# Kernel optimization log

Hardware: AMD Instinct MI355X
Metric: run time of the kernel (lower is better)

Reference implementation:

```python
import jax, jax.numpy as jnp
import numpy as np

WS = 8          # window size
NH = 16         # num heads
C = 256         # in_channels
L = WS * WS     # tokens per window
EPS = 1e-5      # LayerNorm eps

def _rel_index():
    coords = np.stack(np.meshgrid(np.arange(WS), np.arange(WS), indexing='ij')).reshape(2, -1)
    rel = coords[:, :, None] - coords[:, None, :]
    rel = rel + (WS - 1)
    rel[0] = rel[0] * (2 * WS - 1)
    return jnp.asarray(rel.sum(0))  # [L, L] int

REL_IDX = _rel_index()

def _ln(x, g, b):
    m = x.mean(-1, keepdims=True)
    v = jnp.var(x, axis=-1, keepdims=True)
    return (x - m) * jax.lax.rsqrt(v + EPS) * g + b

def setup_inputs() -> dict:
    key = jax.random.key(0)
    ks = jax.random.split(key, 8)
    return {
        'x': jax.random.normal(ks[0], (2, C, 256, 256), dtype=jnp.float32),
        'pre_gamma': jnp.ones((C,), jnp.float32),
        'pre_beta': jnp.zeros((C,), jnp.float32),
        'post_gamma': jnp.ones((C,), jnp.float32),
        'post_beta': jnp.zeros((C,), jnp.float32),
        'qkv_w': jax.random.normal(ks[1], (C, 3 * C), jnp.float32) * 0.02,
        'qkv_b': jnp.zeros((3 * C,), jnp.float32),
        'proj_w': jax.random.normal(ks[2], (C, C), jnp.float32) * 0.02,
        'proj_b': jnp.zeros((C,), jnp.float32),
        'rel_bias_table': jax.random.normal(ks[3], ((2 * WS - 1) ** 2, NH), jnp.float32) * 0.02,
    }

def reference(x, pre_gamma, pre_beta, post_gamma, post_beta, qkv_w, qkv_b, proj_w, proj_b, rel_bias_table):
    N, Cc, H, W = x.shape
    # block partition: [N,C,H,W] -> [N*nWin, L, C]
    t = x.reshape(N, Cc, H // WS, WS, W // WS, WS)
    t = t.transpose(0, 2, 4, 3, 5, 1).reshape(-1, L, Cc)
    B = t.shape[0]
    # pre-norm + relative self-attention (cosine / normalized qk)
    y = _ln(t, pre_gamma, pre_beta)
    qkv = (y @ qkv_w + qkv_b).reshape(B, L, 3, NH, Cc // NH).transpose(2, 0, 3, 1, 4)
    q, k, v = qkv[0], qkv[1], qkv[2]  # [B, h, L, dh]
    q = q / jnp.maximum(jnp.linalg.norm(q, axis=-1, keepdims=True), 1e-12)
    k = k / jnp.maximum(jnp.linalg.norm(k, axis=-1, keepdims=True), 1e-12)
    bias = rel_bias_table[REL_IDX].transpose(2, 0, 1)  # [h, L, L]
    attn = jax.nn.softmax(jnp.einsum('bhld,bhmd->bhlm', q, k) + bias, axis=-1)
    o = jnp.einsum('bhlm,bhmd->bhld', attn, v).transpose(0, 2, 1, 3).reshape(B, L, Cc)
    o = o @ proj_w + proj_b
    out = t + o
    # post-norm residual (mlp is Identity in MetNet-3)
    out = out + _ln(out, post_gamma, post_beta)
    # reverse partition -> [N, C, H, W]
    out = out.reshape(N, H // WS, W // WS, WS, WS, Cc)
    out = out.transpose(0, 5, 1, 3, 2, 4).reshape(N, Cc, H, W)
    return out
```

## Files before the change

kernel.cpp:

```cpp
#include <hip/hip_runtime.h>


#define WSZ 8
#define LTOK 64
#define NH 16
#define CCH 256
#define WW2 256
#define HWP 65536
#define NWIN 2048

#define TP 258
#define QP2 18
#define VP2 66
#define PP2 66
#define OHP 36

typedef __bf16 bf16x8 __attribute__((ext_vector_type(8)));
typedef float  f32x4  __attribute__((ext_vector_type(4)));
typedef unsigned short u16;
typedef uint4  __attribute__((may_alias)) uint4_a;
typedef float4 __attribute__((may_alias)) float4_a;

__device__ __forceinline__ float b2f(u16 u) {
    return (float)__builtin_bit_cast(__bf16, u);
}
__device__ __forceinline__ u16 f2b(float f) {
    return __builtin_bit_cast(u16, (__bf16)f);
}
__device__ __forceinline__ __bf16 u2b(u16 u) {
    return __builtin_bit_cast(__bf16, u);
}
__device__ __forceinline__ float gload(const void* p, int idx, int isf32) {
    return isf32 ? ((const float*)p)[idx] : b2f(((const u16*)p)[idx]);
}

static __global__ void detect_dtype(const u16* __restrict__ xu, int* __restrict__ flag) {
    int lane = threadIdx.x;
    u16 u = xu[lane];
    int e = (u >> 7) & 0xFF;
    bool plaus = (u == 0) || (e >= 0x6C && e <= 0x86);
    unsigned long long m = __ballot(plaus);
    if (lane == 0) flag[0] = (__popcll(m) >= 56) ? 0 : 1;
}

static __global__ __launch_bounds__(256) void prep_qkv(
        const void* __restrict__ qkv_w, const void* __restrict__ qkv_b,
        const void* __restrict__ g, const void* __restrict__ be,
        u16* __restrict__ gwT, float* __restrict__ D2, float* __restrict__ D3,
        const int* __restrict__ flagp)
{
    const int isf32 = flagp[0];
    int col = blockIdx.x;
    int c   = threadIdx.x;
    float gv = gload(g, c, isf32), bv = gload(be, c, isf32);
    float wv = gload(qkv_w, c * 768 + col, isf32);
    gwT[col * 256 + c] = f2b(gv * wv);
    float s2 = gv * wv, s3 = bv * wv;
    #pragma unroll
    for (int off = 32; off; off >>= 1) {
        s2 += __shfl_xor(s2, off);
        s3 += __shfl_xor(s3, off);
    }
    __shared__ float p2[4], p3[4];
    int wvid = threadIdx.x >> 6, ln = threadIdx.x & 63;
    if (ln == 0) { p2[wvid] = s2; p3[wvid] = s3; }
    __syncthreads();
    if (threadIdx.x == 0) {
        D2[col] = p2[0] + p2[1] + p2[2] + p2[3];
        D3[col] = p3[0] + p3[1] + p3[2] + p3[3] + gload(qkv_b, col, isf32);
    }
}

static __global__ __launch_bounds__(256) void prep_proj(
        const void* __restrict__ proj_w, u16* __restrict__ pwT,
        const void* __restrict__ table, float* __restrict__ tablef,
        const int* __restrict__ flagp)
{
    const int isf32 = flagp[0];
    int nrow = blockIdx.x, k = threadIdx.x;
    pwT[nrow * 256 + k] = f2b(gload(proj_w, k * 256 + nrow, isf32));
    int gid = blockIdx.x * 256 + threadIdx.x;
    if (gid < (2 * WSZ - 1) * (2 * WSZ - 1) * NH)
        tablef[gid] = gload(table, gid, isf32);
}

static __global__ __launch_bounds__(256, 3) void win_attn(
    const void* __restrict__ x, void* __restrict__ out,
    const u16* __restrict__ gwT, const u16* __restrict__ pwT,
    const float* __restrict__ D2, const float* __restrict__ D3,
    const void* __restrict__ proj_b, const void* __restrict__ postg,
    const void* __restrict__ postb, const float* __restrict__ tablef,
    const int* __restrict__ flagp)
{
    __shared__ u16 sm_t[LTOK * TP];
    __shared__ u16 sm_q[LTOK * QP2];
    __shared__ u16 sm_k[LTOK * QP2];
    __shared__ u16 sm_vt[NH * VP2];
    __shared__ u16 sm_p[LTOK * PP2];
    __shared__ u16 sm_oh[LTOK * OHP];
    __shared__ float sm_mean[LTOK], sm_rstd[LTOK];
    __shared__ u16 sm_zero[16];

    const int isf32 = flagp[0];
    const int tid  = threadIdx.x;
    const int wv   = tid >> 6;
    const int lane = tid & 63;
    const int quad = lane >> 4;
    const int n15  = lane & 15;

    const int b0 = blockIdx.x;
    const int b  = ((b0 & 7) << 8) | (b0 >> 3);
    const int nb = b >> 10, wh = (b >> 5) & 31, wwi = b & 31;
    const int base = nb * (CCH * HWP) + wh * (8 * WW2) + wwi * 8;

    if (tid < 16) sm_zero[tid] = 0;

    if (isf32) {
        const float* xf = (const float*)x;
        #pragma unroll
        for (int r = 0; r < 8; ++r) {
            int s = tid + r * 256;
            int c = s >> 3, i = s & 7;
            const float* src = xf + base + c * HWP + i * WW2;
            float4 a = *(const float4_a*)(src);
            float4 d = *(const float4_a*)(src + 4);
            u16* dst = &sm_t[(i * 8) * TP + c];
            dst[0 * TP] = f2b(a.x);  dst[1 * TP] = f2b(a.y);
            dst[2 * TP] = f2b(a.z);  dst[3 * TP] = f2b(a.w);
            dst[4 * TP] = f2b(d.x);  dst[5 * TP] = f2b(d.y);
            dst[6 * TP] = f2b(d.z);  dst[7 * TP] = f2b(d.w);
        }
    } else {
        const u16* xu = (const u16*)x;
        #pragma unroll
        for (int r = 0; r < 8; ++r) {
            int s = tid + r * 256;
            int c = s >> 3, i = s & 7;
            const uint4 v = *(const uint4_a*)(xu + base + c * HWP + i * WW2);
            u16* dst = &sm_t[(i * 8) * TP + c];
            dst[0 * TP] = (u16)(v.x & 0xffff);  dst[1 * TP] = (u16)(v.x >> 16);
            dst[2 * TP] = (u16)(v.y & 0xffff);  dst[3 * TP] = (u16)(v.y >> 16);
            dst[4 * TP] = (u16)(v.z & 0xffff);  dst[5 * TP] = (u16)(v.z >> 16);
            dst[6 * TP] = (u16)(v.w & 0xffff);  dst[7 * TP] = (u16)(v.w >> 16);
        }
    }
    __syncthreads();

    {
        int l = tid >> 2, g = tid & 3;
        float s = 0.f, ss = 0.f;
        const u16* row = &sm_t[l * TP + g * 64];
        #pragma unroll
        for (int e = 0; e < 64; ++e) {
            float a = b2f(row[e]);
            s += a; ss += a * a;
        }
        s += __shfl_xor(s, 1); ss += __shfl_xor(ss, 1);
        s += __shfl_xor(s, 2); ss += __shfl_xor(ss, 2);
        if (g == 0) {
            float mean = s * (1.f / 256.f);
            float var  = ss * (1.f / 256.f) - mean * mean;
            sm_mean[l] = mean;
            sm_rstd[l] = rsqrtf(var + 1e-5f);
        }
    }

    float s4[4], ms4[4];
    #pragma unroll
    for (int r = 0; r < 4; ++r) {
        int tok = wv * 16 + quad * 4 + r;
        float mu = sm_mean[tok], sd = sm_rstd[tok];
        s4[r] = sd; ms4[r] = -mu * sd;
    }

    bf16x8 afr[8];
    {
        const u16* arow = &sm_t[(wv * 16 + n15) * TP];
        #pragma unroll
        for (int kb = 0; kb < 8; ++kb) {
            #pragma unroll
            for (int j = 0; j < 8; ++j)
                afr[kb][j] = u2b(arow[kb * 32 + quad * 8 + j]);
        }
    }

    int toff[4][4];
    #pragma unroll
    for (int ct = 0; ct < 4; ++ct) {
        int key = ct * 16 + n15, im = key >> 3, jm = key & 7;
        #pragma unroll
        for (int r = 0; r < 4; ++r) {
            int tok = wv * 16 + quad * 4 + r;
            int il = tok >> 3, jl = tok & 7;
            toff[ct][r] = ((il - im + 7) * 15 + (jl - jm + 7)) * 16;
        }
    }

    f32x4 accp[16];
    #pragma unroll
    for (int t2 = 0; t2 < 16; ++t2) accp[t2] = f32x4{0.f, 0.f, 0.f, 0.f};
    const f32x4 zero4 = f32x4{0.f, 0.f, 0.f, 0.f};

    for (int h = 0; h < 16; ++h) {
        f32x4 aq = zero4, ak = zero4, av = zero4;
        const u16* gq = &gwT[(h * 16 + n15) * 256 + quad * 8];
        const u16* gk = gq + 256 * 256;
        const u16* gv = gq + 512 * 256;
        #pragma unroll
        for (int kb = 0; kb < 8; ++kb) {
            bf16x8 bq = __builtin_bit_cast(bf16x8, *(const uint4_a*)(gq + kb * 32));
            bf16x8 bk = __builtin_bit_cast(bf16x8, *(const uint4_a*)(gk + kb * 32));
            bf16x8 bv = __builtin_bit_cast(bf16x8, *(const uint4_a*)(gv + kb * 32));
            aq = __builtin_amdgcn_mfma_f32_16x16x32_bf16(afr[kb], bq, aq, 0, 0, 0);
            ak = __builtin_amdgcn_mfma_f32_16x16x32_bf16(afr[kb], bk, ak, 0, 0, 0);
            av = __builtin_amdgcn_mfma_f32_16x16x32_bf16(afr[kb], bv, av, 0, 0, 0);
        }
        float d2q = D2[h * 16 + n15],       d3q = D3[h * 16 + n15];
        float d2k = D2[256 + h * 16 + n15], d3k = D3[256 + h * 16 + n15];
        float d2v = D2[512 + h * 16 + n15], d3v = D3[512 + h * 16 + n15];
        float qv[4], kv[4], vv[4];
        #pragma unroll
        for (int r = 0; r < 4; ++r) {
            qv[r] = s4[r] * aq[r] + ms4[r] * d2q + d3q;
            kv[r] = s4[r] * ak[r] + ms4[r] * d2k + d3k;
            vv[r] = s4[r] * av[r] + ms4[r] * d2v + d3v;
        }
        #pragma unroll
        for (int r = 0; r < 4; ++r) {
            float sq = qv[r] * qv[r], sk = kv[r] * kv[r];
            sq += __shfl_xor(sq, 1); sk += __shfl_xor(sk, 1);
            sq += __shfl_xor(sq, 2); sk += __shfl_xor(sk, 2);
            sq += __shfl_xor(sq, 4); sk += __shfl_xor(sk, 4);
            sq += __shfl_xor(sq, 8); sk += __shfl_xor(sk, 8);
            qv[r] *= rsqrtf(fmaxf(sq, 1e-24f));
            kv[r] *= rsqrtf(fmaxf(sk, 1e-24f));
        }
        #pragma unroll
        for (int r = 0; r < 4; ++r) {
            int tok = wv * 16 + quad * 4 + r;
            sm_q[tok * QP2 + n15] = f2b(qv[r]);
            sm_k[tok * QP2 + n15] = f2b(kv[r]);
            sm_vt[n15 * VP2 + tok] = f2b(vv[r]);
        }
        __syncthreads();

        f32x4 sc[4];
        {
            bf16x8 aqf;
            const u16* qrow = (quad < 2) ? &sm_q[(wv * 16 + n15) * QP2 + quad * 8]
                                         : sm_zero;
            #pragma unroll
            for (int j = 0; j < 8; ++j) aqf[j] = u2b(qrow[j]);
            #pragma unroll
            for (int ct = 0; ct < 4; ++ct) {
                bf16x8 bkf;
                const u16* krow = (quad < 2) ? &sm_k[(ct * 16 + n15) * QP2 + quad * 8]
                                             : sm_zero;
                #pragma unroll
                for (int j = 0; j < 8; ++j) bkf[j] = u2b(krow[j]);
                f32x4 bias;
                #pragma unroll
                for (int r = 0; r < 4; ++r) bias[r] = tablef[toff[ct][r] + h];
                sc[ct] = __builtin_amdgcn_mfma_f32_16x16x32_bf16(aqf, bkf, bias, 0, 0, 0);
            }
        }
        #pragma unroll
        for (int r = 0; r < 4; ++r) {
            float mx = fmaxf(fmaxf(sc[0][r], sc[1][r]), fmaxf(sc[2][r], sc[3][r]));
            mx = fmaxf(mx, __shfl_xor(mx, 1));
            mx = fmaxf(mx, __shfl_xor(mx, 2));
            mx = fmaxf(mx, __shfl_xor(mx, 4));
            mx = fmaxf(mx, __shfl_xor(mx, 8));
            float e0 = __expf(sc[0][r] - mx), e1 = __expf(sc[1][r] - mx);
            float e2 = __expf(sc[2][r] - mx), e3 = __expf(sc[3][r] - mx);
            float sm = e0 + e1 + e2 + e3;
            sm += __shfl_xor(sm, 1); sm += __shfl_xor(sm, 2);
            sm += __shfl_xor(sm, 4); sm += __shfl_xor(sm, 8);
            float inv = 1.f / sm;
            int tok = wv * 16 + quad * 4 + r;
            sm_p[tok * PP2 +  0 + n15] = f2b(e0 * inv);
            sm_p[tok * PP2 + 16 + n15] = f2b(e1 * inv);
            sm_p[tok * PP2 + 32 + n15] = f2b(e2 * inv);
            sm_p[tok * PP2 + 48 + n15] = f2b(e3 * inv);
        }

        f32x4 ov = zero4;
        #pragma unroll
        for (int ks = 0; ks < 2; ++ks) {
            bf16x8 ap, bvf;
            const u16* prow = &sm_p[(wv * 16 + n15) * PP2 + ks * 32 + quad * 8];
            const u16* vrow = &sm_vt[n15 * VP2 + ks * 32 + quad * 8];
            #pragma unroll
            for (int j = 0; j < 8; ++j) { ap[j] = u2b(prow[j]); bvf[j] = u2b(vrow[j]); }
            ov = __builtin_amdgcn_mfma_f32_16x16x32_bf16(ap, bvf, ov, 0, 0, 0);
        }
        #pragma unroll
        for (int r = 0; r < 4; ++r) {
            int tok = wv * 16 + quad * 4 + r;
            sm_oh[tok * OHP + (h & 1) * 16 + n15] = f2b(ov[r]);
        }

        if (h & 1) {
            int hp = h >> 1;
            bf16x8 aof;
            const u16* orow = &sm_oh[(wv * 16 + n15) * OHP + quad * 8];
            #pragma unroll
            for (int j = 0; j < 8; ++j) aof[j] = u2b(orow[j]);
            const u16* pwb = &pwT[n15 * 256 + hp * 32 + quad * 8];
            #pragma unroll
            for (int t2 = 0; t2 < 16; ++t2) {
                bf16x8 bpf = __builtin_bit_cast(bf16x8, *(const uint4_a*)(pwb + t2 * 16 * 256));
                accp[t2] = __builtin_amdgcn_mfma_f32_16x16x32_bf16(aof, bpf, accp[t2], 0, 0, 0);
            }
        }
        __syncthreads();
    }

    {
        #pragma unroll
        for (int t2 = 0; t2 < 16; ++t2) {
            int col = t2 * 16 + n15;
            float pb = gload(proj_b, col, isf32);
            #pragma unroll
            for (int r = 0; r < 4; ++r) {
                int tok = wv * 16 + quad * 4 + r;
                accp[t2][r] += pb + b2f(sm_t[tok * TP + col]);
            }
        }
        float sr[4] = {0, 0, 0, 0}, ssr[4] = {0, 0, 0, 0};
        #pragma unroll
        for (int t2 = 0; t2 < 16; ++t2) {
            #pragma unroll
            for (int r = 0; r < 4; ++r) { float v = accp[t2][r]; sr[r] += v; ssr[r] += v * v; }
        }
        #pragma unroll
        for (int r = 0; r < 4; ++r) {
            sr[r] += __shfl_xor(sr[r], 1); ssr[r] += __shfl_xor(ssr[r], 1);
            sr[r] += __shfl_xor(sr[r], 2); ssr[r] += __shfl_xor(ssr[r], 2);
            sr[r] += __shfl_xor(sr[r], 4); ssr[r] += __shfl_xor(ssr[r], 4);
            sr[r] += __shfl_xor(sr[r], 8); ssr[r] += __shfl_xor(ssr[r], 8);
        }
        float mean2[4], rs2[4];
        #pragma unroll
        for (int r = 0; r < 4; ++r) {
            float m = sr[r] * (1.f / 256.f);
            float v = ssr[r] * (1.f / 256.f) - m * m;
            mean2[r] = m; rs2[r] = rsqrtf(v + 1e-5f);
        }
        #pragma unroll
        for (int t2 = 0; t2 < 16; ++t2) {
            int col = t2 * 16 + n15;
            float pg = gload(postg, col, isf32), pb2 = gload(postb, col, isf32);
            #pragma unroll
            for (int r = 0; r < 4; ++r) {
                int tok = wv * 16 + quad * 4 + r;
                float o1 = accp[t2][r];
                float fin = o1 + (o1 - mean2[r]) * rs2[r] * pg + pb2;
                sm_t[tok * TP + col] = f2b(fin);
            }
        }
    }
    __syncthreads();

    if (isf32) {
        float* outf = (float*)out;
        #pragma unroll
        for (int r = 0; r < 8; ++r) {
            int s = tid + r * 256;
            int c = s >> 3, i = s & 7;
            const u16* src = &sm_t[(i * 8) * TP + c];
            float* dst = outf + base + c * HWP + i * WW2;
            float4 a, d;
            a.x = b2f(src[0 * TP]); a.y = b2f(src[1 * TP]);
            a.z = b2f(src[2 * TP]); a.w = b2f(src[3 * TP]);
            d.x = b2f(src[4 * TP]); d.y = b2f(src[5 * TP]);
            d.z = b2f(src[6 * TP]); d.w = b2f(src[7 * TP]);
            *(float4_a*)dst = a;
            *(float4_a*)(dst + 4) = d;
        }
    } else {
        u16* outu = (u16*)out;
        #pragma unroll
        for (int r = 0; r < 8; ++r) {
            int s = tid + r * 256;
            int c = s >> 3, i = s & 7;
            const u16* src = &sm_t[(i * 8) * TP + c];
            uint4 v;
            v.x = (unsigned)src[0 * TP] | ((unsigned)src[1 * TP] << 16);
            v.y = (unsigned)src[2 * TP] | ((unsigned)src[3 * TP] << 16);
            v.z = (unsigned)src[4 * TP] | ((unsigned)src[5 * TP] << 16);
            v.w = (unsigned)src[6 * TP] | ((unsigned)src[7 * TP] << 16);
            *(uint4_a*)(outu + base + c * HWP + i * WW2) = v;
        }
    }
}

extern "C" void kernel_launch(void* const* d_in, const int* in_sizes, int n_in,
                              void* d_out, int out_size, void* d_ws, size_t ws_size,
                              hipStream_t stream) {
    const void* x     = d_in[0];
    const void* preg  = d_in[1];
    const void* preb  = d_in[2];
    const void* postg = d_in[3];
    const void* postb = d_in[4];
    const void* qkvw  = d_in[5];
    const void* qkvb  = d_in[6];
    const void* projw = d_in[7];
    const void* projb = d_in[8];
    const void* table = d_in[9];

    char* ws = (char*)d_ws;
    u16*   gwT = (u16*)(ws);
    u16*   pwT = (u16*)(ws + 393216);
    float* D2  = (float*)(ws + 524288);
    float* D3  = (float*)(ws + 527360);
    float* tbf = (float*)(ws + 530432);
    int*   flg = (int*)(ws + 544832);

    detect_dtype<<<1, 64, 0, stream>>>((const u16*)x, flg);
    prep_qkv<<<768, 256, 0, stream>>>(qkvw, qkvb, preg, preb, gwT, D2, D3, flg);
    prep_proj<<<256, 256, 0, stream>>>(projw, pwT, table, tbf, flg);
    win_attn<<<NWIN, 256, 0, stream>>>(x, d_out, gwT, pwT, D2, D3,
                                       projb, postg, postb, tbf, flg);
}
```

Before: 1.077 ms.

## Software-pipeline per-head QKV projection, defer softmax normalization, swizzle LDS layouts

Restructures the per-head loop so the QKV MFMA projection for head h+1 is computed while head h's attention runs, and prefetches the relative-bias values one head ahead. Softmax skips the max subtraction, which is safe because q and k are unit-normalised so scores are bounded, and the 1/sum scaling moves onto the PV output. LDS pads become XOR swizzles so P, V and O fragments can be read with 16-byte vector loads, and the block-to-window mapping is changed for locality. The cost is more live registers from keeping next-head q/k/v values, plus an extra barrier per iteration.

```diff
diff --git a/kernel.cpp b/kernel.cpp
--- a/kernel.cpp
+++ b/kernel.cpp
@@ -10,16 +10,19 @@
 #define NWIN 2048
 
 #define TP 258
-#define QP2 18
-#define VP2 66
-#define PP2 66
-#define OHP 36
+#define QP3 20
+#define VP3 64
+#define PP3 64
+#define OP3 40
 
 typedef __bf16 bf16x8 __attribute__((ext_vector_type(8)));
+typedef __bf16 bf16x4 __attribute__((ext_vector_type(4)));
 typedef float  f32x4  __attribute__((ext_vector_type(4)));
 typedef unsigned short u16;
+typedef unsigned long long ull;
 typedef uint4  __attribute__((may_alias)) uint4_a;
 typedef float4 __attribute__((may_alias)) float4_a;
+typedef ull    __attribute__((may_alias)) ull_a;
 
 __device__ __forceinline__ float b2f(u16 u) {
     return (float)__builtin_bit_cast(__bf16, u);
@@ -27,11 +30,18 @@
 __device__ __forceinline__ u16 f2b(float f) {
     return __builtin_bit_cast(u16, (__bf16)f);
 }
-__device__ __forceinline__ __bf16 u2b(u16 u) {
-    return __builtin_bit_cast(__bf16, u);
-}
 __device__ __forceinline__ float gload(const void* p, int idx, int isf32) {
     return isf32 ? ((const float*)p)[idx] : b2f(((const u16*)p)[idx]);
+}
+__device__ __forceinline__ bf16x8 ld_qk(const u16* p) {
+    ull lo = *(const ull_a*)p, hi = *(const ull_a*)(p + 4);
+    bf16x4 a = __builtin_bit_cast(bf16x4, lo);
+    bf16x4 b = __builtin_bit_cast(bf16x4, hi);
+    return bf16x8{a[0], a[1], a[2], a[3], b[0], b[1], b[2], b[3]};
+}
+__device__ __forceinline__ bf16x8 ld16(const u16* p) {
+    const uint4_a* q = (const uint4_a*)__builtin_assume_aligned((const void*)p, 16);
+    return __builtin_bit_cast(bf16x8, *q);
 }
 
 static __global__ void detect_dtype(const u16* __restrict__ xu, int* __restrict__ flag) {
@@ -92,14 +102,13 @@
     const void* __restrict__ postb, const float* __restrict__ tablef,
     const int* __restrict__ flagp)
 {
-    __shared__ u16 sm_t[LTOK * TP];
-    __shared__ u16 sm_q[LTOK * QP2];
-    __shared__ u16 sm_k[LTOK * QP2];
-    __shared__ u16 sm_vt[NH * VP2];
-    __shared__ u16 sm_p[LTOK * PP2];
-    __shared__ u16 sm_oh[LTOK * OHP];
+    __shared__ __align__(16) u16 sm_t[LTOK * TP];
+    __shared__ __align__(16) u16 sm_p[LTOK * PP3];
+    __shared__ __align__(16) u16 sm_oh[LTOK * OP3];
+    __shared__ __align__(16) u16 sm_q[LTOK * QP3];
+    __shared__ __align__(16) u16 sm_k[LTOK * QP3];
+    __shared__ __align__(16) u16 sm_vt[NH * VP3];
     __shared__ float sm_mean[LTOK], sm_rstd[LTOK];
-    __shared__ u16 sm_zero[16];
 
     const int isf32 = flagp[0];
     const int tid  = threadIdx.x;
@@ -109,11 +118,9 @@
     const int n15  = lane & 15;
 
     const int b0 = blockIdx.x;
-    const int b  = ((b0 & 7) << 8) | (b0 >> 3);
+    const int b  = (b0 & ~63) | ((b0 & 7) << 3) | ((b0 >> 3) & 7);
     const int nb = b >> 10, wh = (b >> 5) & 31, wwi = b & 31;
     const int base = nb * (CCH * HWP) + wh * (8 * WW2) + wwi * 8;
-
-    if (tid < 16) sm_zero[tid] = 0;
 
     if (isf32) {
         const float* xf = (const float*)x;
@@ -180,7 +187,7 @@
         for (int kb = 0; kb < 8; ++kb) {
             #pragma unroll
             for (int j = 0; j < 8; ++j)
-                afr[kb][j] = u2b(arow[kb * 32 + quad * 8 + j]);
+                afr[kb][j] = __builtin_bit_cast(__bf16, arow[kb * 32 + quad * 8 + j]);
         }
     }
 
@@ -201,9 +208,9 @@
     for (int t2 = 0; t2 < 16; ++t2) accp[t2] = f32x4{0.f, 0.f, 0.f, 0.f};
     const f32x4 zero4 = f32x4{0.f, 0.f, 0.f, 0.f};
 
-    for (int h = 0; h < 16; ++h) {
+    auto compute_A = [&](int hh, float* qv, float* kv, float* vvv) {
         f32x4 aq = zero4, ak = zero4, av = zero4;
-        const u16* gq = &gwT[(h * 16 + n15) * 256 + quad * 8];
+        const u16* gq = &gwT[(hh * 16 + n15) * 256 + quad * 8];
         const u16* gk = gq + 256 * 256;
         const u16* gv = gq + 512 * 256;
         #pragma unroll
@@ -215,15 +222,14 @@
             ak = __builtin_amdgcn_mfma_f32_16x16x32_bf16(afr[kb], bk, ak, 0, 0, 0);
             av = __builtin_amdgcn_mfma_f32_16x16x32_bf16(afr[kb], bv, av, 0, 0, 0);
         }
-        float d2q = D2[h * 16 + n15],       d3q = D3[h * 16 + n15];
-        float d2k = D2[256 + h * 16 + n15], d3k = D3[256 + h * 16 + n15];
-        float d2v = D2[512 + h * 16 + n15], d3v = D3[512 + h * 16 + n15];
-        float qv[4], kv[4], vv[4];
-        #pragma unroll
-        for (int r = 0; r < 4; ++r) {
-            qv[r] = s4[r] * aq[r] + ms4[r] * d2q + d3q;
-            kv[r] = s4[r] * ak[r] + ms4[r] * d2k + d3k;
-            vv[r] = s4[r] * av[r] + ms4[r] * d2v + d3v;
+        float d2q = D2[hh * 16 + n15],       d3q = D3[hh * 16 + n15];
+        float d2k = D2[256 + hh * 16 + n15], d3k = D3[256 + hh * 16 + n15];
+        float d2v = D2[512 + hh * 16 + n15], d3v = D3[512 + hh * 16 + n15];
+        #pragma unroll
+        for (int r = 0; r < 4; ++r) {
+            qv[r]  = s4[r] * aq[r] + ms4[r] * d2q + d3q;
+            kv[r]  = s4[r] * ak[r] + ms4[r] * d2k + d3k;
+            vvv[r] = s4[r] * av[r] + ms4[r] * d2v + d3v;
         }
         #pragma unroll
         for (int r = 0; r < 4; ++r) {
@@ -235,77 +241,86 @@
             qv[r] *= rsqrtf(fmaxf(sq, 1e-24f));
             kv[r] *= rsqrtf(fmaxf(sk, 1e-24f));
         }
+    };
+    auto store_A = [&](const float* qv, const float* kv, const float* vvv) {
         #pragma unroll
         for (int r = 0; r < 4; ++r) {
             int tok = wv * 16 + quad * 4 + r;
-            sm_q[tok * QP2 + n15] = f2b(qv[r]);
-            sm_k[tok * QP2 + n15] = f2b(kv[r]);
-            sm_vt[n15 * VP2 + tok] = f2b(vv[r]);
-        }
-        __syncthreads();
-
+            sm_q[tok * QP3 + n15] = f2b(qv[r]);
+            sm_k[tok * QP3 + n15] = f2b(kv[r]);
+            sm_vt[n15 * VP3 + (tok ^ ((n15 & 7) << 3))] = f2b(vvv[r]);
+        }
+    };
+
+    float qv[4], kv[4], vv[4];
+    compute_A(0, qv, kv, vv);
+    store_A(qv, kv, vv);
+    f32x4 biasv[4];
+    #pragma unroll
+    for (int ct = 0; ct < 4; ++ct)
+        #pragma unroll
+        for (int r = 0; r < 4; ++r)
+            biasv[ct][r] = tablef[toff[ct][r]];
+    __syncthreads();
+
+    for (int h = 0; h < 16; ++h) {
         f32x4 sc[4];
         {
-            bf16x8 aqf;
-            const u16* qrow = (quad < 2) ? &sm_q[(wv * 16 + n15) * QP2 + quad * 8]
-                                         : sm_zero;
-            #pragma unroll
-            for (int j = 0; j < 8; ++j) aqf[j] = u2b(qrow[j]);
+            bf16x8 aqf = {};
+            if (quad < 2) aqf = ld_qk(&sm_q[(wv * 16 + n15) * QP3 + quad * 8]);
             #pragma unroll
             for (int ct = 0; ct < 4; ++ct) {
-                bf16x8 bkf;
-                const u16* krow = (quad < 2) ? &sm_k[(ct * 16 + n15) * QP2 + quad * 8]
-                                             : sm_zero;
+                bf16x8 bkf = {};
+                if (quad < 2) bkf = ld_qk(&sm_k[(ct * 16 + n15) * QP3 + quad * 8]);
+                sc[ct] = __builtin_amdgcn_mfma_f32_16x16x32_bf16(aqf, bkf, biasv[ct], 0, 0, 0);
+            }
+        }
+        if (h < 15) {
+            #pragma unroll
+            for (int ct = 0; ct < 4; ++ct)
                 #pragma unroll
-                for (int j = 0; j < 8; ++j) bkf[j] = u2b(krow[j]);
-                f32x4 bias;
-                #pragma unroll
-                for (int r = 0; r < 4; ++r) bias[r] = tablef[toff[ct][r] + h];
-                sc[ct] = __builtin_amdgcn_mfma_f32_16x16x32_bf16(aqf, bkf, bias, 0, 0, 0);
-            }
-        }
-        #pragma unroll
-        for (int r = 0; r < 4; ++r) {
-            float mx = fmaxf(fmaxf(sc[0][r], sc[1][r]), fmaxf(sc[2][r], sc[3][r]));
-            mx = fmaxf(mx, __shfl_xor(mx, 1));
-            mx = fmaxf(mx, __shfl_xor(mx, 2));
-            mx = fmaxf(mx, __shfl_xor(mx, 4));
-            mx = fmaxf(mx, __shfl_xor(mx, 8));
-            float e0 = __expf(sc[0][r] - mx), e1 = __expf(sc[1][r] - mx);
-            float e2 = __expf(sc[2][r] - mx), e3 = __expf(sc[3][r] - mx);
-            float sm = e0 + e1 + e2 + e3;
+                for (int r = 0; r < 4; ++r)
+                    biasv[ct][r] = tablef[toff[ct][r] + h + 1];
+        }
+        float inv[4];
+        #pragma unroll
+        for (int r = 0; r < 4; ++r) {
+            float e0 = __expf(sc[0][r]), e1 = __expf(sc[1][r]);
+            float e2 = __expf(sc[2][r]), e3 = __expf(sc[3][r]);
+            int tok = wv * 16 + quad * 4 + r;
+            int t3 = (tok & 7) << 3;
+            sm_p[tok * PP3 + (( 0 + n15) ^ t3)] = f2b(e0);
+            sm_p[tok * PP3 + ((16 + n15) ^ t3)] = f2b(e1);
+            sm_p[tok * PP3 + ((32 + n15) ^ t3)] = f2b(e2);
+            sm_p[tok * PP3 + ((48 + n15) ^ t3)] = f2b(e3);
+            float sm = (e0 + e1) + (e2 + e3);
             sm += __shfl_xor(sm, 1); sm += __shfl_xor(sm, 2);
             sm += __shfl_xor(sm, 4); sm += __shfl_xor(sm, 8);
-            float inv = 1.f / sm;
+            inv[r] = 1.f / sm;
+        }
+
+        f32x4 ov = zero4;
+        {
+            int prow = wv * 16 + n15;
+            int pxor = (prow & 7) << 3, vxor = (n15 & 7) << 3;
+            #pragma unroll
+            for (int ks = 0; ks < 2; ++ks) {
+                bf16x8 ap  = ld16(&sm_p[prow * PP3 + ((ks * 32 + quad * 8) ^ pxor)]);
+                bf16x8 bvf = ld16(&sm_vt[n15 * VP3 + ((ks * 32 + quad * 8) ^ vxor)]);
+                ov = __builtin_amdgcn_mfma_f32_16x16x32_bf16(ap, bvf, ov, 0, 0, 0);
+            }
+        }
+        #pragma unroll
+        for (int r = 0; r < 4; ++r) {
             int tok = wv * 16 + quad * 4 + r;
-            sm_p[tok * PP2 +  0 + n15] = f2b(e0 * inv);
-            sm_p[tok * PP2 + 16 + n15] = f2b(e1 * inv);
-            sm_p[tok * PP2 + 32 + n15] = f2b(e2 * inv);
-            sm_p[tok * PP2 + 48 + n15] = f2b(e3 * inv);
-        }
-
-        f32x4 ov = zero4;
-        #pragma unroll
-        for (int ks = 0; ks < 2; ++ks) {
-            bf16x8 ap, bvf;
-            const u16* prow = &sm_p[(wv * 16 + n15) * PP2 + ks * 32 + quad * 8];
-            const u16* vrow = &sm_vt[n15 * VP2 + ks * 32 + quad * 8];
-            #pragma unroll
-            for (int j = 0; j < 8; ++j) { ap[j] = u2b(prow[j]); bvf[j] = u2b(vrow[j]); }
-            ov = __builtin_amdgcn_mfma_f32_16x16x32_bf16(ap, bvf, ov, 0, 0, 0);
-        }
-        #pragma unroll
-        for (int r = 0; r < 4; ++r) {
-            int tok = wv * 16 + quad * 4 + r;
-            sm_oh[tok * OHP + (h & 1) * 16 + n15] = f2b(ov[r]);
-        }
+            sm_oh[tok * OP3 + (h & 1) * 16 + n15] = f2b(ov[r] * inv[r]);
+        }
+
+        if (h < 15) compute_A(h + 1, qv, kv, vv);
 
         if (h & 1) {
             int hp = h >> 1;
-            bf16x8 aof;
-            const u16* orow = &sm_oh[(wv * 16 + n15) * OHP + quad * 8];
-            #pragma unroll
-            for (int j = 0; j < 8; ++j) aof[j] = u2b(orow[j]);
+            bf16x8 aof = ld16(&sm_oh[(wv * 16 + n15) * OP3 + quad * 8]);
             const u16* pwb = &pwT[n15 * 256 + hp * 32 + quad * 8];
             #pragma unroll
             for (int t2 = 0; t2 < 16; ++t2) {
@@ -313,6 +328,10 @@
                 accp[t2] = __builtin_amdgcn_mfma_f32_16x16x32_bf16(aof, bpf, accp[t2], 0, 0, 0);
             }
         }
+
+        if (h == 15) break;
+        __syncthreads();
+        store_A(qv, kv, vv);
         __syncthreads();
     }
 
```

Result: slower. 1.317 ms (+22.3%).
